# Kernel tuning notes

Measured on AMD Instinct MI355X. Metric: run time of the kernel, lower is better.

The kernel has to match this reference:

```python
import jax, jax.numpy as jnp
import numpy as np
import math

B, L, D = 2, 2048, 1024
H = 16
DH = D // H  # 64
XPOS_SCALE_BASE = 512.0
THETA = 10000.0


def setup_inputs() -> dict:
    key = jax.random.key(0)
    ks = jax.random.split(key, 9)
    s = 0.02  # keep logits in a sane range like trained weights
    return {
        "x": jax.random.normal(ks[0], (B, L, D), dtype=jnp.float32),
        "Wq": jax.random.normal(ks[1], (D, D), dtype=jnp.float32) * s,
        "bq": jax.random.normal(ks[2], (D,), dtype=jnp.float32) * s,
        "Wk": jax.random.normal(ks[3], (D, D), dtype=jnp.float32) * s,
        "bk": jax.random.normal(ks[4], (D,), dtype=jnp.float32) * s,
        "Wv": jax.random.normal(ks[5], (D, D), dtype=jnp.float32) * s,
        "bv": jax.random.normal(ks[6], (D,), dtype=jnp.float32) * s,
        "Wo": jax.random.normal(ks[7], (D, D), dtype=jnp.float32) * s,
        "bo": jax.random.normal(ks[8], (D,), dtype=jnp.float32) * s,
    }


def _rotate_half(t):
    # pairwise interleaved rotation, as in rotary_embedding_torch
    t1 = t[..., 0::2]
    t2 = t[..., 1::2]
    return jnp.stack([-t2, t1], axis=-1).reshape(t.shape)


def _xpos_rotate(q, k):
    # q, k: [B, H, L, DH]; xPos rotary embedding (use_xpos=True)
    seq = q.shape[2]
    half = jnp.arange(0, DH, 2, dtype=jnp.float32)
    inv_freq = 1.0 / (THETA ** (half / DH))            # [DH/2]
    t = jnp.arange(seq, dtype=jnp.float32)             # [L]
    freqs = t[:, None] * inv_freq[None, :]             # [L, DH/2]
    freqs = jnp.repeat(freqs, 2, axis=-1)              # [L, DH] interleaved
    # xPos length-extrapolatable scale
    scale_vec = (half + 0.4 * DH) / (1.4 * DH)         # [DH/2]
    power = (t - seq // 2) / XPOS_SCALE_BASE           # [L]
    scale = scale_vec[None, :] ** power[:, None]       # [L, DH/2]
    scale = jnp.repeat(scale, 2, axis=-1)              # [L, DH]
    cos = jnp.cos(freqs)
    sin = jnp.sin(freqs)
    q_out = q * (cos * scale) + _rotate_half(q) * (sin * scale)
    k_out = k * (cos / scale) + _rotate_half(k) * (sin / scale)
    return q_out, k_out


def reference(x, Wq, bq, Wk, bk, Wv, bv, Wo, bo):
    b, l, d = x.shape
    # projections; note source swaps names: v_mat <- k-proj, k_mat <- v-proj
    q = (x @ Wq.T + bq).reshape(b, l, H, DH).transpose(0, 2, 1, 3)  # [b,h,l,dh]
    v = (x @ Wk.T + bk).reshape(b, l, H, DH).transpose(0, 2, 1, 3)
    k = (x @ Wv.T + bv).reshape(b, l, H, DH).transpose(0, 2, 1, 3)
    q, k = _xpos_rotate(q, k)
    # source divides by sqrt(Dh * num_heads) == sqrt(dim)
    scores = jnp.einsum("bhqd,bhkd->bhqk", q, k) / math.sqrt(d)
    weights = jax.nn.softmax(scores, axis=-1)
    inter = jnp.einsum("bhqk,bhkd->bhqd", weights, v)
    inter = inter.transpose(0, 2, 1, 3).reshape(b, l, d)
    return inter @ Wo.T + bo
```

## Files before the change

kernel.cpp:

```cpp
#include <hip/hip_runtime.h>
#include <math.h>

#define NB 2
#define NL 2048
#define ND 1024
#define NH 16
#define NDH 64
#define NBL 4096

typedef __attribute__((ext_vector_type(4))) float f32x4;
typedef __attribute__((ext_vector_type(8))) short s16x8;

__device__ __forceinline__ unsigned short f2bf(float f){
  unsigned int u = __float_as_uint(f);
  u += 0x7FFF + ((u >> 16) & 1);
  return (unsigned short)(u >> 16);
}

__global__ void cvt_all(const float* __restrict__ x,
                        const float* __restrict__ wq, const float* __restrict__ wk,
                        const float* __restrict__ wv, const float* __restrict__ wo,
                        unsigned short* __restrict__ xb,
                        unsigned short* __restrict__ wqb, unsigned short* __restrict__ wkb,
                        unsigned short* __restrict__ wvb, unsigned short* __restrict__ wob){
  int i = blockIdx.x * blockDim.x + threadIdx.x;
  const float* s; unsigned short* d; int off;
  if (i < (1<<20)) { s = x; d = xb; off = i; }
  else {
    int j = i - (1<<20); int w = j >> 18; off = j & ((1<<18)-1);
    s = (w==0)?wq:(w==1)?wk:(w==2)?wv:wo;
    d = (w==0)?wqb:(w==1)?wkb:(w==2)?wvb:wob;
  }
  float4 f = reinterpret_cast<const float4*>(s)[off];
  ushort4 r; r.x=f2bf(f.x); r.y=f2bf(f.y); r.z=f2bf(f.z); r.w=f2bf(f.w);
  reinterpret_cast<ushort4*>(d)[off] = r;
}

__global__ void rope_tables(float* __restrict__ cosT, float* __restrict__ sinT, float* __restrict__ scT){
  int t = blockIdx.x * blockDim.x + threadIdx.x;
  int l = t >> 5, i = t & 31;
  float half = 2.0f * (float)i;
  float inv_freq = 1.0f / powf(10000.0f, half / 64.0f);
  float fr = (float)l * inv_freq;
  float sv = (half + 0.4f * 64.0f) / (1.4f * 64.0f);
  float pw = ((float)l - 1024.0f) / 512.0f;
  cosT[t] = cosf(fr);
  sinT[t] = sinf(fr);
  scT[t]  = powf(sv, pw);
}

__device__ __forceinline__ void gemm_core128(
    const unsigned short* __restrict__ A, const unsigned short* __restrict__ W,
    int row0, int col0,
    unsigned short (&As)[128][32], unsigned short (&Bs)[128][32],
    f32x4 (&acc)[4][4])
{
  const int tid  = threadIdx.x;
  const int wave = tid >> 6, lane = tid & 63;
  const int m16  = lane & 15, quad = lane >> 4;
  const int mrow = (wave & 1) * 64, ncol = (wave >> 1) * 64;
  const int rA   = lane >> 2, cA = (lane & 3) * 8;

  for (int k0 = 0; k0 < ND; k0 += 32){
    __syncthreads();
#pragma unroll
    for (int i2 = 0; i2 < 2; i2++){
      const int c = wave * 2 + i2;
      const unsigned short* ga = A + (size_t)(row0 + c*16 + rA) * ND + k0 + cA;
      const unsigned short* gb = W + (size_t)(col0 + c*16 + rA) * ND + k0 + cA;
      __builtin_amdgcn_global_load_lds((const __attribute__((address_space(1))) void*)ga,
                                       (__attribute__((address_space(3))) void*)&As[c*16][0], 16, 0, 0);
      __builtin_amdgcn_global_load_lds((const __attribute__((address_space(1))) void*)gb,
                                       (__attribute__((address_space(3))) void*)&Bs[c*16][0], 16, 0, 0);
    }
    __syncthreads();
    s16x8 af[4], bf[4];
#pragma unroll
    for (int mt = 0; mt < 4; mt++) af[mt] = *reinterpret_cast<const s16x8*>(&As[mrow + mt*16 + m16][quad*8]);
#pragma unroll
    for (int nt = 0; nt < 4; nt++) bf[nt] = *reinterpret_cast<const s16x8*>(&Bs[ncol + nt*16 + m16][quad*8]);
#pragma unroll
    for (int mt = 0; mt < 4; mt++)
#pragma unroll
      for (int nt = 0; nt < 4; nt++)
        acc[mt][nt] = __builtin_amdgcn_mfma_f32_16x16x32_bf16(af[mt], bf[nt], acc[mt][nt], 0, 0, 0);
  }
}

__global__ __launch_bounds__(256) void gemm_qkv(
    const unsigned short* __restrict__ A,
    const unsigned short* __restrict__ Wq, const float* __restrict__ bq,
    const unsigned short* __restrict__ Wk, const float* __restrict__ bk,
    const unsigned short* __restrict__ Wv, const float* __restrict__ bv,
    unsigned short* __restrict__ qb, unsigned short* __restrict__ kb,
    unsigned short* __restrict__ vtb,
    const float* __restrict__ cosT, const float* __restrict__ sinT, const float* __restrict__ scT)
{
  __shared__ unsigned short As[128][32];
  __shared__ unsigned short Bs[128][32];
  __shared__ unsigned short T[128][72];

  const int mode = blockIdx.z;
  const unsigned short* W = (mode==0) ? Wq : (mode==1) ? Wk : Wv;
  const float* bias       = (mode==0) ? bq : (mode==1) ? bk : bv;

  const int row0 = blockIdx.x * 128, col0 = blockIdx.y * 128;
  f32x4 acc[4][4] = {};
  gemm_core128(A, W, row0, col0, As, Bs, acc);

  const int tid  = threadIdx.x;
  const int wave = tid >> 6, lane = tid & 63;
  const int m16  = lane & 15, quad = lane >> 4;
  const int mrow = (wave & 1) * 64, ncol = (wave >> 1) * 64;

  if (mode == 2){
    const int b = row0 >> 11, l0 = row0 & (NL - 1);
#pragma unroll
    for (int h2 = 0; h2 < 2; h2++){
      __syncthreads();
      if ((wave >> 1) == h2){
#pragma unroll
        for (int mt = 0; mt < 4; mt++)
#pragma unroll
          for (int nt = 0; nt < 4; nt++)
#pragma unroll
            for (int r = 0; r < 4; r++){
              int lrow = mrow + mt*16 + quad*4 + r;
              int dh   = nt*16 + m16;
              T[lrow][dh] = f2bf(acc[mt][nt][r] + bias[col0 + h2*64 + dh]);
            }
      }
      __syncthreads();
      const int bh = b * NH + (col0 >> 6) + h2;
#pragma unroll
      for (int j4 = 0; j4 < 4; j4++){
        int c = tid * 4 + j4;
        int d = c >> 4, seg = (c & 15) * 8;
        unsigned short tmp[8];
#pragma unroll
        for (int jj = 0; jj < 8; jj++) tmp[jj] = T[seg + jj][d];
        *reinterpret_cast<uint4*>(vtb + (size_t)(bh * NDH + d) * NL + l0 + seg) =
            *reinterpret_cast<uint4*>(tmp);
      }
    }
  } else {
    const float qscale = (mode == 0) ? 0.03125f : 1.0f;
    unsigned short* dst = (mode == 0) ? qb : kb;
#pragma unroll
    for (int mt = 0; mt < 4; mt++)
#pragma unroll
      for (int nt = 0; nt < 4; nt++)
#pragma unroll
        for (int r = 0; r < 4; r++){
          int grow = row0 + mrow + mt*16 + quad*4 + r;
          int gcol = col0 + ncol + nt*16 + m16;
          float v = acc[mt][nt][r] + bias[gcol];
          int b = grow >> 11, l = grow & (NL - 1);
          int h = gcol >> 6, dh = gcol & 63;
          float pv = __shfl_xor(v, 1);
          int ti = l*32 + (dh >> 1);
          float cs = cosT[ti], sn = sinT[ti], sc = scT[ti];
          if (mode == 1) sc = 1.0f / sc;
          float rh = (dh & 1) ? pv : -pv;
          float ov = (v * cs + rh * sn) * sc * qscale;
          dst[(((size_t)(b * NH + h)) * NL + l) * NDH + dh] = f2bf(ov);
        }
  }
}

__global__ __launch_bounds__(256) void gemm_o(
    const unsigned short* __restrict__ A, const unsigned short* __restrict__ W,
    const float* __restrict__ bias, float* __restrict__ out)
{
  __shared__ unsigned short As[128][32];
  __shared__ unsigned short Bs[128][32];
  const int row0 = blockIdx.x * 128, col0 = blockIdx.y * 128;
  f32x4 acc[4][4] = {};
  gemm_core128(A, W, row0, col0, As, Bs, acc);

  const int tid  = threadIdx.x;
  const int wave = tid >> 6, lane = tid & 63;
  const int m16  = lane & 15, quad = lane >> 4;
  const int mrow = (wave & 1) * 64, ncol = (wave >> 1) * 64;
#pragma unroll
  for (int mt = 0; mt < 4; mt++)
#pragma unroll
    for (int nt = 0; nt < 4; nt++)
#pragma unroll
      for (int r = 0; r < 4; r++){
        int grow = row0 + mrow + mt*16 + quad*4 + r;
        int gcol = col0 + ncol + nt*16 + m16;
        out[(size_t)grow * ND + gcol] = acc[mt][nt][r] + bias[gcol];
      }
}

__global__ __launch_bounds__(256) void attn_kernel(
    const unsigned short* __restrict__ qb,
    const unsigned short* __restrict__ kb,
    const unsigned short* __restrict__ vtb,
    unsigned short* __restrict__ ob)
{
  __shared__ unsigned short Qs[64][72];
  __shared__ unsigned short Ks[64][72];
  __shared__ unsigned short Vs[64][72];
  __shared__ unsigned short Ps[64][72];

  const int tid  = threadIdx.x;
  const int wave = tid >> 6, lane = tid & 63;
  const int m16  = lane & 15, quad = lane >> 4;
  const int bh   = blockIdx.y;
  const int q0   = blockIdx.x * 64;
  const unsigned short* Q  = qb  + (size_t)bh * NL * NDH;
  const unsigned short* K  = kb  + (size_t)bh * NL * NDH;
  const unsigned short* Vt = vtb + (size_t)bh * NDH * NL;

#pragma unroll
  for (int it = 0; it < 2; it++){
    int idx = tid + it*256;
    int r = idx >> 3, sg = (idx & 7) * 8;
    *reinterpret_cast<uint4*>(&Qs[r][sg]) =
        *reinterpret_cast<const uint4*>(Q + (size_t)(q0 + r) * NDH + sg);
  }

  float lsum[4] = {0, 0, 0, 0};
  f32x4 o[4] = {{0,0,0,0},{0,0,0,0},{0,0,0,0},{0,0,0,0}};

  for (int kt = 0; kt < 32; kt++){
    __syncthreads();
    const int k0 = kt * 64;
#pragma unroll
    for (int it = 0; it < 2; it++){
      int idx = tid + it*256;
      int r = idx >> 3, sg = (idx & 7) * 8;
      *reinterpret_cast<uint4*>(&Ks[r][sg]) =
          *reinterpret_cast<const uint4*>(K + (size_t)(k0 + r) * NDH + sg);
      *reinterpret_cast<uint4*>(&Vs[r][sg]) =
          *reinterpret_cast<const uint4*>(Vt + (size_t)r * NL + k0 + sg);
    }
    __syncthreads();

    f32x4 s[4] = {{0,0,0,0},{0,0,0,0},{0,0,0,0},{0,0,0,0}};
#pragma unroll
    for (int ks = 0; ks < 2; ks++){
      s16x8 a = *reinterpret_cast<const s16x8*>(&Qs[wave*16 + m16][ks*32 + quad*8]);
#pragma unroll
      for (int nt = 0; nt < 4; nt++){
        s16x8 b = *reinterpret_cast<const s16x8*>(&Ks[nt*16 + m16][ks*32 + quad*8]);
        s[nt] = __builtin_amdgcn_mfma_f32_16x16x32_bf16(a, b, s[nt], 0, 0, 0);
      }
    }

#pragma unroll
    for (int nt = 0; nt < 4; nt++){
#pragma unroll
      for (int r = 0; r < 4; r++){
        float pv = __expf(s[nt][r]);
        lsum[r] += pv;
        Ps[wave*16 + quad*4 + r][nt*16 + m16] = f2bf(pv);
      }
    }

#pragma unroll
    for (int ks = 0; ks < 2; ks++){
      s16x8 a = *reinterpret_cast<const s16x8*>(&Ps[wave*16 + m16][ks*32 + quad*8]);
#pragma unroll
      for (int nt = 0; nt < 4; nt++){
        s16x8 b = *reinterpret_cast<const s16x8*>(&Vs[nt*16 + m16][ks*32 + quad*8]);
        o[nt] = __builtin_amdgcn_mfma_f32_16x16x32_bf16(a, b, o[nt], 0, 0, 0);
      }
    }
  }

  float linv[4];
#pragma unroll
  for (int r = 0; r < 4; r++){
    float t = lsum[r];
#pragma unroll
    for (int off = 1; off < 16; off <<= 1) t += __shfl_xor(t, off, 16);
    linv[r] = 1.0f / t;
  }
  const int bb = bh >> 4, h = bh & 15;
#pragma unroll
  for (int nt = 0; nt < 4; nt++){
#pragma unroll
    for (int r = 0; r < 4; r++){
      const int row = q0 + wave*16 + quad*4 + r;
      ob[((size_t)(bb * NL + row)) * ND + h * NDH + nt*16 + m16] = f2bf(o[nt][r] * linv[r]);
    }
  }
}

extern "C" void kernel_launch(void* const* d_in, const int* in_sizes, int n_in,
                              void* d_out, int out_size, void* d_ws, size_t ws_size,
                              hipStream_t stream)
{
  (void)in_sizes; (void)n_in; (void)out_size; (void)ws_size;
  const float* x  = (const float*)d_in[0];
  const float* Wq = (const float*)d_in[1];
  const float* bq = (const float*)d_in[2];
  const float* Wk = (const float*)d_in[3];
  const float* bk = (const float*)d_in[4];
  const float* Wv = (const float*)d_in[5];
  const float* bv = (const float*)d_in[6];
  const float* Wo = (const float*)d_in[7];
  const float* bo = (const float*)d_in[8];
  float* out = (float*)d_out;

  char* p = (char*)d_ws;
  unsigned short* xb   = (unsigned short*)p; p += (size_t)NBL*ND*2;
  unsigned short* wqb  = (unsigned short*)p; p += (size_t)ND*ND*2;
  unsigned short* wkb  = (unsigned short*)p; p += (size_t)ND*ND*2;
  unsigned short* wvb  = (unsigned short*)p; p += (size_t)ND*ND*2;
  unsigned short* wob  = (unsigned short*)p; p += (size_t)ND*ND*2;
  unsigned short* qbuf = (unsigned short*)p; p += (size_t)NBL*ND*2;
  unsigned short* kbuf = (unsigned short*)p; p += (size_t)NBL*ND*2;
  unsigned short* vtb  = (unsigned short*)p; p += (size_t)NBL*ND*2;
  unsigned short* ibuf = (unsigned short*)p; p += (size_t)NBL*ND*2;
  float* cosT = (float*)p; p += (size_t)NL*32*4;
  float* sinT = (float*)p; p += (size_t)NL*32*4;
  float* scT  = (float*)p; p += (size_t)NL*32*4;

  hipLaunchKernelGGL(cvt_all, dim3(8192), dim3(256), 0, stream,
                     x, Wq, Wk, Wv, Wo, xb, wqb, wkb, wvb, wob);
  hipLaunchKernelGGL(rope_tables, dim3(NL*32/256), dim3(256), 0, stream, cosT, sinT, scT);

  hipLaunchKernelGGL(gemm_qkv, dim3(NBL/128, ND/128, 3), dim3(256), 0, stream,
                     xb, wqb, bq, wvb, bv, wkb, bk, qbuf, kbuf, vtb, cosT, sinT, scT);

  hipLaunchKernelGGL(attn_kernel, dim3(NL/64, NB*NH), dim3(256), 0, stream,
                     qbuf, kbuf, vtb, ibuf);

  hipLaunchKernelGGL(gemm_o, dim3(NBL/128, ND/128), dim3(256), 0, stream, ibuf, wob, bo, out);
}
```

Measured before the change: 243.6 us.

## Enlarge attention query tile, hold Q in registers, retile output GEMM

The attention kernel now processes 128 queries per block, with each wave handling 32 queries. Q fragments stay in registers, and S is computed transposed (K as A operand) so that P can be written with packed bf16 stores. The normalised output is staged through shared memory for coalesced 16-byte global writes. The output projection GEMM switches to 128x64 tiles using direct global-to-LDS loads, which doubles the block count. This aims to cut LDS traffic and improve occupancy, at the cost of higher register pressure and fewer attention blocks.

```diff
diff --git a/kernel.cpp b/kernel.cpp
--- a/kernel.cpp
+++ b/kernel.cpp
@@ -15,6 +15,11 @@
   unsigned int u = __float_as_uint(f);
   u += 0x7FFF + ((u >> 16) & 1);
   return (unsigned short)(u >> 16);
+}
+
+__device__ __forceinline__ unsigned int pk2bf(float lo, float hi){
+  return __builtin_amdgcn_perm(__float_as_uint(hi) + 0x8000u,
+                               __float_as_uint(lo) + 0x8000u, 0x07060302u);
 }
 
 __global__ void cvt_all(const float* __restrict__ x,
@@ -173,19 +178,44 @@
     const float* __restrict__ bias, float* __restrict__ out)
 {
   __shared__ unsigned short As[128][32];
-  __shared__ unsigned short Bs[128][32];
-  const int row0 = blockIdx.x * 128, col0 = blockIdx.y * 128;
-  f32x4 acc[4][4] = {};
-  gemm_core128(A, W, row0, col0, As, Bs, acc);
-
+  __shared__ unsigned short Bs[64][32];
   const int tid  = threadIdx.x;
   const int wave = tid >> 6, lane = tid & 63;
   const int m16  = lane & 15, quad = lane >> 4;
-  const int mrow = (wave & 1) * 64, ncol = (wave >> 1) * 64;
+  const int mrow = (wave & 1) * 64, ncol = (wave >> 1) * 32;
+  const int rA   = lane >> 2, cA = (lane & 3) * 8;
+  const int row0 = blockIdx.x * 128, col0 = blockIdx.y * 64;
+
+  f32x4 acc[4][2] = {};
+
+  for (int k0 = 0; k0 < ND; k0 += 32){
+    __syncthreads();
+#pragma unroll
+    for (int i3 = 0; i3 < 3; i3++){
+      const int c = wave * 3 + i3;
+      const unsigned short* g; unsigned short* l;
+      if (c < 8){ g = A + (size_t)(row0 + c*16 + rA) * ND + k0 + cA;      l = &As[c*16][0]; }
+      else      { g = W + (size_t)(col0 + (c-8)*16 + rA) * ND + k0 + cA;  l = &Bs[(c-8)*16][0]; }
+      __builtin_amdgcn_global_load_lds((const __attribute__((address_space(1))) void*)g,
+                                       (__attribute__((address_space(3))) void*)l, 16, 0, 0);
+    }
+    __syncthreads();
+    s16x8 af[4], bf[2];
+#pragma unroll
+    for (int mt = 0; mt < 4; mt++) af[mt] = *reinterpret_cast<const s16x8*>(&As[mrow + mt*16 + m16][quad*8]);
+#pragma unroll
+    for (int nt = 0; nt < 2; nt++) bf[nt] = *reinterpret_cast<const s16x8*>(&Bs[ncol + nt*16 + m16][quad*8]);
+#pragma unroll
+    for (int mt = 0; mt < 4; mt++)
+#pragma unroll
+      for (int nt = 0; nt < 2; nt++)
+        acc[mt][nt] = __builtin_amdgcn_mfma_f32_16x16x32_bf16(af[mt], bf[nt], acc[mt][nt], 0, 0, 0);
+  }
+
 #pragma unroll
   for (int mt = 0; mt < 4; mt++)
 #pragma unroll
-    for (int nt = 0; nt < 4; nt++)
+    for (int nt = 0; nt < 2; nt++)
 #pragma unroll
       for (int r = 0; r < 4; r++){
         int grow = row0 + mrow + mt*16 + quad*4 + r;
@@ -194,36 +224,35 @@
       }
 }
 
-__global__ __launch_bounds__(256) void attn_kernel(
+__global__ __launch_bounds__(256, 2) void attn_kernel(
     const unsigned short* __restrict__ qb,
     const unsigned short* __restrict__ kb,
     const unsigned short* __restrict__ vtb,
     unsigned short* __restrict__ ob)
 {
-  __shared__ unsigned short Qs[64][72];
   __shared__ unsigned short Ks[64][72];
   __shared__ unsigned short Vs[64][72];
-  __shared__ unsigned short Ps[64][72];
+  __shared__ unsigned short Ps[128][72];
 
   const int tid  = threadIdx.x;
   const int wave = tid >> 6, lane = tid & 63;
   const int m16  = lane & 15, quad = lane >> 4;
   const int bh   = blockIdx.y;
-  const int q0   = blockIdx.x * 64;
+  const int q0   = blockIdx.x * 128;
   const unsigned short* Q  = qb  + (size_t)bh * NL * NDH;
   const unsigned short* K  = kb  + (size_t)bh * NL * NDH;
   const unsigned short* Vt = vtb + (size_t)bh * NDH * NL;
 
-#pragma unroll
-  for (int it = 0; it < 2; it++){
-    int idx = tid + it*256;
-    int r = idx >> 3, sg = (idx & 7) * 8;
-    *reinterpret_cast<uint4*>(&Qs[r][sg]) =
-        *reinterpret_cast<const uint4*>(Q + (size_t)(q0 + r) * NDH + sg);
-  }
-
-  float lsum[4] = {0, 0, 0, 0};
-  f32x4 o[4] = {{0,0,0,0},{0,0,0,0},{0,0,0,0},{0,0,0,0}};
+  s16x8 qf[2][2];
+#pragma unroll
+  for (int qt = 0; qt < 2; qt++)
+#pragma unroll
+    for (int ks = 0; ks < 2; ks++)
+      qf[qt][ks] = *reinterpret_cast<const s16x8*>(
+          Q + (size_t)(q0 + wave*32 + qt*16 + m16) * NDH + ks*32 + quad*8);
+
+  float ls[2] = {0.f, 0.f};
+  f32x4 ot[4][2] = {};
 
   for (int kt = 0; kt < 32; kt++){
     __syncthreads();
@@ -239,55 +268,81 @@
     }
     __syncthreads();
 
-    f32x4 s[4] = {{0,0,0,0},{0,0,0,0},{0,0,0,0},{0,0,0,0}};
-#pragma unroll
-    for (int ks = 0; ks < 2; ks++){
-      s16x8 a = *reinterpret_cast<const s16x8*>(&Qs[wave*16 + m16][ks*32 + quad*8]);
-#pragma unroll
-      for (int nt = 0; nt < 4; nt++){
-        s16x8 b = *reinterpret_cast<const s16x8*>(&Ks[nt*16 + m16][ks*32 + quad*8]);
-        s[nt] = __builtin_amdgcn_mfma_f32_16x16x32_bf16(a, b, s[nt], 0, 0, 0);
-      }
-    }
-
-#pragma unroll
-    for (int nt = 0; nt < 4; nt++){
-#pragma unroll
-      for (int r = 0; r < 4; r++){
-        float pv = __expf(s[nt][r]);
-        lsum[r] += pv;
-        Ps[wave*16 + quad*4 + r][nt*16 + m16] = f2bf(pv);
-      }
-    }
-
-#pragma unroll
-    for (int ks = 0; ks < 2; ks++){
-      s16x8 a = *reinterpret_cast<const s16x8*>(&Ps[wave*16 + m16][ks*32 + quad*8]);
-#pragma unroll
-      for (int nt = 0; nt < 4; nt++){
-        s16x8 b = *reinterpret_cast<const s16x8*>(&Vs[nt*16 + m16][ks*32 + quad*8]);
-        o[nt] = __builtin_amdgcn_mfma_f32_16x16x32_bf16(a, b, o[nt], 0, 0, 0);
-      }
-    }
-  }
-
-  float linv[4];
-#pragma unroll
-  for (int r = 0; r < 4; r++){
-    float t = lsum[r];
-#pragma unroll
-    for (int off = 1; off < 16; off <<= 1) t += __shfl_xor(t, off, 16);
-    linv[r] = 1.0f / t;
-  }
+    s16x8 kf[4][2], vf[4][2];
+#pragma unroll
+    for (int mt = 0; mt < 4; mt++)
+#pragma unroll
+      for (int ks = 0; ks < 2; ks++){
+        kf[mt][ks] = *reinterpret_cast<const s16x8*>(&Ks[mt*16 + m16][ks*32 + quad*8]);
+        vf[mt][ks] = *reinterpret_cast<const s16x8*>(&Vs[mt*16 + m16][ks*32 + quad*8]);
+      }
+
+    f32x4 st[2][4] = {};
+#pragma unroll
+    for (int qt = 0; qt < 2; qt++)
+#pragma unroll
+      for (int mt = 0; mt < 4; mt++)
+#pragma unroll
+        for (int ks = 0; ks < 2; ks++)
+          st[qt][mt] = __builtin_amdgcn_mfma_f32_16x16x32_bf16(kf[mt][ks], qf[qt][ks], st[qt][mt], 0, 0, 0);
+
+#pragma unroll
+    for (int qt = 0; qt < 2; qt++){
+#pragma unroll
+      for (int mt = 0; mt < 4; mt++){
+        float e0 = __expf(st[qt][mt][0]);
+        float e1 = __expf(st[qt][mt][1]);
+        float e2 = __expf(st[qt][mt][2]);
+        float e3 = __expf(st[qt][mt][3]);
+        ls[qt] += (e0 + e1) + (e2 + e3);
+        uint2 pk; pk.x = pk2bf(e0, e1); pk.y = pk2bf(e2, e3);
+        *reinterpret_cast<uint2*>(&Ps[wave*32 + qt*16 + m16][mt*16 + quad*4]) = pk;
+      }
+    }
+
+    s16x8 pf[2][2];
+#pragma unroll
+    for (int qt = 0; qt < 2; qt++)
+#pragma unroll
+      for (int ks = 0; ks < 2; ks++)
+        pf[qt][ks] = *reinterpret_cast<const s16x8*>(&Ps[wave*32 + qt*16 + m16][ks*32 + quad*8]);
+#pragma unroll
+    for (int mt = 0; mt < 4; mt++)
+#pragma unroll
+      for (int qt = 0; qt < 2; qt++)
+#pragma unroll
+        for (int ks = 0; ks < 2; ks++)
+          ot[mt][qt] = __builtin_amdgcn_mfma_f32_16x16x32_bf16(vf[mt][ks], pf[qt][ks], ot[mt][qt], 0, 0, 0);
+  }
+
+  float linv[2];
+#pragma unroll
+  for (int qt = 0; qt < 2; qt++){
+    float t = ls[qt];
+    t += __shfl_xor(t, 16);
+    t += __shfl_xor(t, 32);
+    linv[qt] = 1.0f / t;
+  }
+
+#pragma unroll
+  for (int mt = 0; mt < 4; mt++)
+#pragma unroll
+    for (int qt = 0; qt < 2; qt++){
+      float o0 = ot[mt][qt][0] * linv[qt];
+      float o1 = ot[mt][qt][1] * linv[qt];
+      float o2 = ot[mt][qt][2] * linv[qt];
+      float o3 = ot[mt][qt][3] * linv[qt];
+      uint2 pk; pk.x = pk2bf(o0, o1); pk.y = pk2bf(o2, o3);
+      *reinterpret_cast<uint2*>(&Ps[wave*32 + qt*16 + m16][mt*16 + quad*4]) = pk;
+    }
+  __syncthreads();
+
   const int bb = bh >> 4, h = bh & 15;
-#pragma unroll
-  for (int nt = 0; nt < 4; nt++){
-#pragma unroll
-    for (int r = 0; r < 4; r++){
-      const int row = q0 + wave*16 + quad*4 + r;
-      ob[((size_t)(bb * NL + row)) * ND + h * NDH + nt*16 + m16] = f2bf(o[nt][r] * linv[r]);
-    }
-  }
+  const int row = tid >> 1, half = tid & 1;
+  unsigned short* dst = ob + ((size_t)(bb*NL + q0 + row)) * ND + h*NDH + half*32;
+#pragma unroll
+  for (int j = 0; j < 4; j++)
+    *reinterpret_cast<uint4*>(dst + j*8) = *reinterpret_cast<const uint4*>(&Ps[row][half*32 + j*8]);
 }
 
 extern "C" void kernel_launch(void* const* d_in, const int* in_sizes, int n_in,
@@ -327,8 +382,8 @@
   hipLaunchKernelGGL(gemm_qkv, dim3(NBL/128, ND/128, 3), dim3(256), 0, stream,
                      xb, wqb, bq, wvb, bv, wkb, bk, qbuf, kbuf, vtb, cosT, sinT, scT);
 
-  hipLaunchKernelGGL(attn_kernel, dim3(NL/64, NB*NH), dim3(256), 0, stream,
+  hipLaunchKernelGGL(attn_kernel, dim3(NL/128, NB*NH), dim3(256), 0, stream,
                      qbuf, kbuf, vtb, ibuf);
 
-  hipLaunchKernelGGL(gemm_o, dim3(NBL/128, ND/128), dim3(256), 0, stream, ibuf, wob, bo, out);
-}
+  hipLaunchKernelGGL(gemm_o, dim3(NBL/128, ND/64), dim3(256), 0, stream, ibuf, wob, bo, out);
+}
```

Measured after the change: 224.4 us. -7.9%, faster.
